# Optimization experiments

Measured on AMD Instinct MI355X. Metric: run time of the kernel, lower is better.

## Reference

```python
import jax, jax.numpy as jnp
import numpy as np

H = 128          # hidden_dim
L = 3            # num_layers
EPS = 1e-5       # BatchNorm eps


def setup_inputs() -> dict:
    key = jax.random.key(0)
    ks = jax.random.split(key, 12)
    B, N = 32, 8192
    s = 0.05
    x = jax.random.normal(ks[0], (B, N, 2), dtype=jnp.float32)
    mask = jnp.ones((B, N), dtype=jnp.float32)
    # parameters, stored as [in, out]
    emb_w = jax.random.normal(ks[1], (2, H), jnp.float32) * s
    emb_b = jnp.zeros((H,), jnp.float32)
    lin_w = jax.random.normal(ks[2], (L, H, H), jnp.float32) * s
    lin_b = jnp.zeros((L, H), jnp.float32)
    nb_w = jax.random.normal(ks[3], (L, H, H), jnp.float32) * s
    nb_b = jnp.zeros((L, H), jnp.float32)
    bn_g = jnp.ones((L, H), jnp.float32)
    bn_b = jnp.zeros((L, H), jnp.float32)
    out1_w = jax.random.normal(ks[4], (H, H // 2), jnp.float32) * s
    out1_b = jnp.zeros((H // 2,), jnp.float32)
    out2_w = jax.random.normal(ks[5], (H // 2, 2), jnp.float32) * s
    out2_b = jnp.zeros((2,), jnp.float32)
    return dict(x=x, mask=mask, emb_w=emb_w, emb_b=emb_b,
                lin_w=lin_w, lin_b=lin_b, nb_w=nb_w, nb_b=nb_b,
                bn_g=bn_g, bn_b=bn_b, out1_w=out1_w, out1_b=out1_b,
                out2_w=out2_w, out2_b=out2_b)


def reference(x, mask, emb_w, emb_b, lin_w, lin_b, nb_w, nb_b,
              bn_g, bn_b, out1_w, out1_b, out2_w, out2_b):
    m = mask[..., None]                     # [B, N, 1]
    h = x @ emb_w + emb_b                   # [B, N, H]
    for i in range(L):
        # graph conv: self transform + ring-neighbor (roll) transform
        nsum = jnp.roll(h, 1, axis=1) + jnp.roll(h, -1, axis=1)
        h_new = (h @ lin_w[i] + lin_b[i] + nsum @ nb_w[i] + nb_b[i]) * m
        # BatchNorm1d (training-mode batch stats over batch*nodes per channel)
        mean = jnp.mean(h_new, axis=(0, 1))
        var = jnp.mean(jnp.square(h_new - mean), axis=(0, 1))  # biased var
        h_new = (h_new - mean) * jax.lax.rsqrt(var + EPS) * bn_g[i] + bn_b[i]
        h_new = jax.nn.relu(h_new)          # dropout treated as identity (eval)
        h = h + h_new                       # residual
    out = jax.nn.relu(h @ out1_w + out1_b) @ out2_w + out2_b  # [B, N, 2]
    return out * m
```

## Files before the change

### kernel.cpp

```cpp
#include <hip/hip_runtime.h>
#include <cstddef>

#define H      128
#define NBATCH 32
#define NN     8192
#define RTOT   (NBATCH*NN)
#define NLAYER 3
#define BNEPS  1e-5f
#define NSLOT  16
#define CNPB   128
#define NTILEC (RTOT/CNPB)
#define HNPB   64
#define HS_STRIDE 136

typedef _Float16 f16;
typedef __attribute__((ext_vector_type(8))) _Float16 half8;
typedef __attribute__((ext_vector_type(4))) float f32x4;

__device__ __forceinline__ void unpackh8(uint4 pk, float* d) {
    const f16* hp = (const f16*)&pk;
    #pragma unroll
    for (int i = 0; i < 8; ++i) d[i] = (float)hp[i];
}
__device__ __forceinline__ uint4 packh8(const float* s) {
    uint4 pk;
    f16* hp = (f16*)&pk;
    #pragma unroll
    for (int i = 0; i < 8; ++i) hp[i] = (f16)s[i];
    return pk;
}

__device__ __forceinline__ void load_bfrags(
    const f16* __restrict__ Wt, half8 bW[2][4], int colbase, int l15, int quad)
{
    #pragma unroll
    for (int nt = 0; nt < 2; ++nt) {
        int nrow = colbase + nt * 16 + l15;
        #pragma unroll
        for (int ks = 0; ks < 4; ++ks)
            bW[nt][ks] = *((const half8*)(Wt + nrow * 128 + ks * 32 + quad * 8));
    }
}

__device__ __forceinline__ void conv_mfma8(
    const f16* __restrict__ hs, const half8 bWl[2][4], const half8 bWn[2][4],
    f32x4 acc[8][2], int l15, int quad)
{
    #pragma unroll
    for (int mt = 0; mt < 8; ++mt) {
        acc[mt][0] = (f32x4){0.f, 0.f, 0.f, 0.f};
        acc[mt][1] = (f32x4){0.f, 0.f, 0.f, 0.f};
    }
    #pragma unroll
    for (int ks = 0; ks < 4; ++ks) {
        #pragma unroll
        for (int mt = 0; mt < 8; ++mt) {
            int row = mt * 16 + l15;
            const f16* base = hs + row * HS_STRIDE + ks * 32 + quad * 8;
            half8 hm = *((const half8*)(base + HS_STRIDE));
            half8 hd = *((const half8*)(base));
            half8 hu = *((const half8*)(base + 2 * HS_STRIDE));
            half8 an = hd + hu;
            acc[mt][0] = __builtin_amdgcn_mfma_f32_16x16x32_f16(hm, bWl[0][ks], acc[mt][0], 0, 0, 0);
            acc[mt][1] = __builtin_amdgcn_mfma_f32_16x16x32_f16(hm, bWl[1][ks], acc[mt][1], 0, 0, 0);
            acc[mt][0] = __builtin_amdgcn_mfma_f32_16x16x32_f16(an, bWn[0][ks], acc[mt][0], 0, 0, 0);
            acc[mt][1] = __builtin_amdgcn_mfma_f32_16x16x32_f16(an, bWn[1][ks], acc[mt][1], 0, 0, 0);
        }
    }
}

__global__ __launch_bounds__(256) void k_prep(
    const float* __restrict__ lin_w, const float* __restrict__ nb_w,
    f16* __restrict__ Wlt, f16* __restrict__ Wnt)
{
    int id = blockIdx.x * 256 + threadIdx.x;
    int mat = id / 49152;
    int r   = id - mat * 49152;
    int l   = r >> 14;
    int r2  = r & 16383;
    int k   = r2 >> 7;
    int n   = r2 & 127;
    const float* src = mat ? nb_w : lin_w;
    f16*         dst = mat ? Wnt  : Wlt;
    dst[l * 16384 + n * 128 + k] = (f16)src[l * 16384 + k * 128 + n];
}

__device__ __forceinline__ void conv_epilogue_c(
    f32x4 acc[8][2], const float bsum[2], const float* __restrict__ msk,
    f16* __restrict__ hnb, float* __restrict__ gstats,
    int tile, int wave, int quad, int lane, int slot)
{
    uint2* out2 = (uint2*)hnb;
    float s[2] = {0.f, 0.f}, ss[2] = {0.f, 0.f};
    #pragma unroll
    for (int nt = 0; nt < 2; ++nt) {
        #pragma unroll
        for (int mt = 0; mt < 8; ++mt) {
            f16 v4[4];
            #pragma unroll
            for (int reg = 0; reg < 4; ++reg) {
                int lrow = mt * 16 + quad * 4 + reg;
                float v = (acc[mt][nt][reg] + bsum[nt]) * msk[lrow];
                v4[reg] = (f16)v;
                s[nt] += v; ss[nt] += v * v;
            }
            size_t chunk = ((size_t)tile * 4 + wave) * 16 + mt * 2 + nt;
            out2[chunk * 64 + lane] = *((const uint2*)v4);
        }
    }
    #pragma unroll
    for (int nt = 0; nt < 2; ++nt) {
        s[nt]  += __shfl_xor(s[nt], 16);  s[nt]  += __shfl_xor(s[nt], 32);
        ss[nt] += __shfl_xor(ss[nt], 16); ss[nt] += __shfl_xor(ss[nt], 32);
    }
    if (lane < 16) {
        int colbase = wave * 32;
        #pragma unroll
        for (int nt = 0; nt < 2; ++nt) {
            int col = colbase + nt * 16 + lane;
            atomicAdd(&gstats[slot * 2 * H + col],     s[nt]);
            atomicAdd(&gstats[slot * 2 * H + H + col], ss[nt]);
        }
    }
}

__global__ __launch_bounds__(256) void k_conv0f(
    const float* __restrict__ x, const float* __restrict__ ew,
    const float* __restrict__ eb,
    const f16* __restrict__ Wlt, const f16* __restrict__ Wnt,
    const float* __restrict__ bl, const float* __restrict__ bnb,
    const float* __restrict__ mask,
    f16* __restrict__ hnb, float* __restrict__ gstats)
{
    __shared__ __align__(16) f16 hs[(CNPB + 2) * HS_STRIDE];
    __shared__ float ews[3 * H], msk[CNPB];
    const int t = threadIdx.x, lane = t & 63;
    const int l15 = lane & 15, quad = lane >> 4;
    const int wave = t >> 6;
    const int colbase = wave * 32;
    const int r0 = blockIdx.x * CNPB;
    const int batch = r0 >> 13, n0 = r0 & (NN - 1);

    half8 bWl[2][4], bWn[2][4];
    load_bfrags(Wlt, bWl, colbase, l15, quad);
    load_bfrags(Wnt, bWn, colbase, l15, quad);
    float bsum[2];
    #pragma unroll
    for (int nt = 0; nt < 2; ++nt) {
        int col = colbase + nt * 16 + l15;
        bsum[nt] = bl[col] + bnb[col];
    }
    for (int c = t; c < H; c += 256) {
        ews[c] = ew[c]; ews[H + c] = ew[H + c]; ews[2 * H + c] = eb[c];
    }
    if (t < CNPB) msk[t] = mask[r0 + t];
    __syncthreads();

    for (int i = t; i < (CNPB + 2) * 16; i += 256) {
        int row = i >> 4, g = i & 15;
        int n = (n0 + row - 1 + NN) & (NN - 1);
        const float* xp = x + 2 * ((size_t)batch * NN + n);
        float x0 = xp[0], x1 = xp[1];
        f16 o[8];
        #pragma unroll
        for (int e = 0; e < 8; ++e) {
            int c = g * 8 + e;
            o[e] = (f16)fmaf(x1, ews[H + c], fmaf(x0, ews[c], ews[2 * H + c]));
        }
        *((uint4*)(hs + row * HS_STRIDE + g * 8)) = *((const uint4*)o);
    }
    __syncthreads();

    f32x4 acc[8][2];
    conv_mfma8(hs, bWl, bWn, acc, l15, quad);

    conv_epilogue_c(acc, bsum, msk, hnb, gstats,
                    blockIdx.x, wave, quad, lane, blockIdx.x & (NSLOT - 1));
}

__global__ __launch_bounds__(256) void k_conv(
    const f16* __restrict__ hb,
    const f16* __restrict__ Wlt, const f16* __restrict__ Wnt,
    const float* __restrict__ bl, const float* __restrict__ bnb,
    const float* __restrict__ mask,
    f16* __restrict__ hnb, float* __restrict__ gstats)
{
    __shared__ __align__(16) f16 hs[(CNPB + 2) * HS_STRIDE];
    __shared__ float msk[CNPB];
    const int t = threadIdx.x, lane = t & 63;
    const int l15 = lane & 15, quad = lane >> 4;
    const int wave = t >> 6;
    const int colbase = wave * 32;
    const int r0 = blockIdx.x * CNPB;
    const int batch = r0 >> 13, n0 = r0 & (NN - 1);

    half8 bWl[2][4], bWn[2][4];
    load_bfrags(Wlt, bWl, colbase, l15, quad);
    load_bfrags(Wnt, bWn, colbase, l15, quad);
    float bsum[2];
    #pragma unroll
    for (int nt = 0; nt < 2; ++nt) {
        int col = colbase + nt * 16 + l15;
        bsum[nt] = bl[col] + bnb[col];
    }
    if (t < CNPB) msk[t] = mask[r0 + t];

    for (int i = t; i < (CNPB + 2) * 16; i += 256) {
        int row = i >> 4, g = i & 15;
        int n = (n0 + row - 1 + NN) & (NN - 1);
        *((uint4*)(hs + row * HS_STRIDE + g * 8)) =
            *((const uint4*)(hb + ((size_t)(batch * NN + n)) * H + g * 8));
    }
    __syncthreads();

    f32x4 acc[8][2];
    conv_mfma8(hs, bWl, bWn, acc, l15, quad);

    conv_epilogue_c(acc, bsum, msk, hnb, gstats,
                    blockIdx.x, wave, quad, lane, blockIdx.x & (NSLOT - 1));
}

__device__ __forceinline__ void norm_ingest(
    const f16* __restrict__ hnb, int blk, int t,
    const float* __restrict__ scl_s, const float* __restrict__ sft_s,
    f16* __restrict__ g)
{
    const uint4* src = (const uint4*)hnb + (size_t)blk * 2048;
    for (int i = t; i < 2048; i += 256) {
        uint4 pk = src[i];
        int chunk = i >> 5;
        int L     = (i & 31) * 2;
        int ntv   = chunk & 1;
        int mtv   = (chunk >> 1) & 7;
        int wv    = chunk >> 4;
        int c0    = wv * 32 + ntv * 16 + (L & 15);
        int row0  = mtv * 16 + (L >> 4) * 4;
        float vv[8];
        unpackh8(pk, vv);
        #pragma unroll
        for (int e = 0; e < 8; ++e) {
            int cc = c0 + (e >> 2);
            int rr = row0 + (e & 3);
            float q = fmaxf(fmaf(vv[e], scl_s[cc], sft_s[cc]), 0.f);
            g[rr * HS_STRIDE + cc] = (f16)q;
        }
    }
}

__device__ __forceinline__ void bn_finalize(
    const float* __restrict__ gstats, const float* __restrict__ bn_g,
    const float* __restrict__ bn_b, int t, float* scl_s, float* sft_s)
{
    if (t < H) {
        float s = 0.f, ss = 0.f;
        #pragma unroll
        for (int i = 0; i < NSLOT; ++i) {
            s  += gstats[i * 2 * H + t];
            ss += gstats[i * 2 * H + H + t];
        }
        const float invR = 1.f / (float)RTOT;
        float mean = s * invR;
        float var  = ss * invR - mean * mean;
        float inv  = rsqrtf(var + BNEPS);
        float sc   = bn_g[t] * inv;
        scl_s[t] = sc;
        sft_s[t] = fmaf(-mean, sc, bn_b[t]);
    }
}

__global__ __launch_bounds__(256) void k_norm0(
    const float* __restrict__ x, const float* __restrict__ ew,
    const float* __restrict__ eb, const f16* __restrict__ hnb,
    const float* __restrict__ gstats, const float* __restrict__ bn_g,
    const float* __restrict__ bn_b, f16* __restrict__ hb)
{
    __shared__ __align__(16) f16 g[CNPB * HS_STRIDE];
    __shared__ float scl_s[H], sft_s[H], ews[3 * H];
    const int t = threadIdx.x;
    const int blk = blockIdx.x;
    const size_t r0 = (size_t)blk * CNPB;

    bn_finalize(gstats, bn_g, bn_b, t, scl_s, sft_s);
    if (t < H) { ews[t] = ew[t]; ews[H + t] = ew[H + t]; ews[2 * H + t] = eb[t]; }
    __syncthreads();

    norm_ingest(hnb, blk, t, scl_s, sft_s, g);
    __syncthreads();

    for (int i = t; i < 2048; i += 256) {
        int row = i >> 4, gg = i & 15;
        size_t grow = r0 + row;
        float x0 = x[2 * grow], x1 = x[2 * grow + 1];
        uint4 pg = *((const uint4*)(g + row * HS_STRIDE + gg * 8));
        float vg[8], vh[8];
        unpackh8(pg, vg);
        #pragma unroll
        for (int e = 0; e < 8; ++e) {
            int c = gg * 8 + e;
            float h0 = fmaf(x1, ews[H + c], fmaf(x0, ews[c], ews[2 * H + c]));
            vh[e] = h0 + vg[e];
        }
        *((uint4*)(hb + grow * H + gg * 8)) = packh8(vh);
    }
}

__global__ __launch_bounds__(256) void k_norm(
    const f16* __restrict__ hnb, const float* __restrict__ gstats,
    const float* __restrict__ bn_g, const float* __restrict__ bn_b,
    f16* __restrict__ hb)
{
    __shared__ __align__(16) f16 g[CNPB * HS_STRIDE];
    __shared__ float scl_s[H], sft_s[H];
    const int t = threadIdx.x;
    const int blk = blockIdx.x;
    const size_t r0 = (size_t)blk * CNPB;

    bn_finalize(gstats, bn_g, bn_b, t, scl_s, sft_s);
    __syncthreads();

    norm_ingest(hnb, blk, t, scl_s, sft_s, g);
    __syncthreads();

    for (int i = t; i < 2048; i += 256) {
        int row = i >> 4, gg = i & 15;
        size_t grow = r0 + row;
        uint4 ph = *((const uint4*)(hb + grow * H + gg * 8));
        uint4 pg = *((const uint4*)(g + row * HS_STRIDE + gg * 8));
        float vh[8], vg[8];
        unpackh8(ph, vh);
        unpackh8(pg, vg);
        #pragma unroll
        for (int e = 0; e < 8; ++e) vh[e] += vg[e];
        *((uint4*)(hb + grow * H + gg * 8)) = packh8(vh);
    }
}

__global__ __launch_bounds__(256) void k_head(
    const f16* __restrict__ hb, const float* __restrict__ W1,
    const float* __restrict__ b1, const float* __restrict__ W2,
    const float* __restrict__ b2, const float* __restrict__ mask,
    float* __restrict__ out)
{
    __shared__ f16 hs [64 * HS_STRIDE];
    __shared__ f16 w1t[64 * HS_STRIDE];
    const int t    = threadIdx.x;
    const int wave = t >> 6;
    const int lane = t & 63;
    const int l15  = lane & 15;
    const int quad = lane >> 4;
    const int r0   = blockIdx.x * HNPB;

    for (int i = t; i < 64 * 16; i += 256) {
        int row = i >> 4, g = i & 15;
        *((uint4*)(hs + row * HS_STRIDE + g * 8)) =
            *((const uint4*)(hb + (size_t)(r0 + row) * H + g * 8));
    }
    for (int i = t; i < H * 64; i += 256) {
        int k = i >> 6, n = i & 63;
        w1t[n * HS_STRIDE + k] = (f16)W1[i];
    }
    __syncthreads();

    f32x4 acc[4];
    #pragma unroll
    for (int nt = 0; nt < 4; ++nt) acc[nt] = (f32x4){0.f, 0.f, 0.f, 0.f};

    #pragma unroll
    for (int ks = 0; ks < 4; ++ks) {
        half8 a = *((const half8*)(hs + (wave * 16 + l15) * HS_STRIDE + ks * 32 + quad * 8));
        #pragma unroll
        for (int nt = 0; nt < 4; ++nt) {
            half8 b = *((const half8*)(w1t + (nt * 16 + l15) * HS_STRIDE + ks * 32 + quad * 8));
            acc[nt] = __builtin_amdgcn_mfma_f32_16x16x32_f16(a, b, acc[nt], 0, 0, 0);
        }
    }

    float p0[4] = {0,0,0,0}, p1[4] = {0,0,0,0};
    #pragma unroll
    for (int nt = 0; nt < 4; ++nt) {
        int col = nt * 16 + l15;
        float bb = b1[col];
        float wa = W2[2 * col], wb = W2[2 * col + 1];
        #pragma unroll
        for (int reg = 0; reg < 4; ++reg) {
            float v = fmaxf(acc[nt][reg] + bb, 0.f);
            p0[reg] = fmaf(v, wa, p0[reg]);
            p1[reg] = fmaf(v, wb, p1[reg]);
        }
    }
    #pragma unroll
    for (int reg = 0; reg < 4; ++reg) {
        p0[reg] += __shfl_xor(p0[reg], 1); p0[reg] += __shfl_xor(p0[reg], 2);
        p0[reg] += __shfl_xor(p0[reg], 4); p0[reg] += __shfl_xor(p0[reg], 8);
        p1[reg] += __shfl_xor(p1[reg], 1); p1[reg] += __shfl_xor(p1[reg], 2);
        p1[reg] += __shfl_xor(p1[reg], 4); p1[reg] += __shfl_xor(p1[reg], 8);
    }
    if (l15 == 0) {
        #pragma unroll
        for (int reg = 0; reg < 4; ++reg) {
            int gr = r0 + wave * 16 + quad * 4 + reg;
            float m = mask[gr];
            float2 o;
            o.x = (p0[reg] + b2[0]) * m;
            o.y = (p1[reg] + b2[1]) * m;
            *((float2*)(out + 2 * gr)) = o;
        }
    }
}

extern "C" void kernel_launch(void* const* d_in, const int* in_sizes, int n_in,
                              void* d_out, int out_size, void* d_ws, size_t ws_size,
                              hipStream_t stream)
{
    const float* x     = (const float*)d_in[0];
    const float* mask  = (const float*)d_in[1];
    const float* emb_w = (const float*)d_in[2];
    const float* emb_b = (const float*)d_in[3];
    const float* lin_w = (const float*)d_in[4];
    const float* lin_b = (const float*)d_in[5];
    const float* nb_w  = (const float*)d_in[6];
    const float* nb_b  = (const float*)d_in[7];
    const float* bn_g  = (const float*)d_in[8];
    const float* bn_b  = (const float*)d_in[9];
    const float* o1w   = (const float*)d_in[10];
    const float* o1b   = (const float*)d_in[11];
    const float* o2w   = (const float*)d_in[12];
    const float* o2b   = (const float*)d_in[13];
    float* out = (float*)d_out;

    char* ws = (char*)d_ws;
    f16* hb  = (f16*)ws;
    f16* hnb = (f16*)(ws + (size_t)RTOT * H * 2);

    float* gst = (float*)d_out;
    f16* Wlt = (f16*)((float*)d_out + 65536);
    f16* Wnt = Wlt + NLAYER * H * H;

    hipMemsetAsync(gst, 0, NLAYER * NSLOT * 2 * H * sizeof(float), stream);
    k_prep<<<384, 256, 0, stream>>>(lin_w, nb_w, Wlt, Wnt);

    k_conv0f<<<NTILEC, 256, 0, stream>>>(
        x, emb_w, emb_b, Wlt, Wnt, lin_b, nb_b, mask, hnb, gst);
    k_norm0<<<NTILEC, 256, 0, stream>>>(
        x, emb_w, emb_b, hnb, gst, bn_g, bn_b, hb);

    for (int i = 1; i < NLAYER; ++i) {
        k_conv<<<NTILEC, 256, 0, stream>>>(
            hb, Wlt + i * H * H, Wnt + i * H * H,
            lin_b + i * H, nb_b + i * H, mask,
            hnb, gst + i * NSLOT * 2 * H);
        k_norm<<<NTILEC, 256, 0, stream>>>(
            hnb, gst + i * NSLOT * 2 * H, bn_g + i * H, bn_b + i * H, hb);
    }
    k_head<<<RTOT / HNPB, 256, 0, stream>>>(hb, o1w, o1b, o2w, o2b, mask, out);
}
```

Baseline: 343.6 us.

## Fuse BatchNorm apply and residual into next conv's load and head

Removes the separate normalize kernels. Each conv kernel now rebuilds its input tile from the previous pre-norm activations and a tiny per-channel scale/shift buffer computed by a one-block finalize kernel. The epilogue stages results through shared memory to write row-major tiles with coalesced stores. This saves a full read and write pass per layer. In exchange, halo rows are recomputed, and the path needs a third workspace buffer, so it only runs when the workspace size check passes.

```diff
diff --git a/kernel.cpp b/kernel.cpp
--- a/kernel.cpp
+++ b/kernel.cpp
@@ -124,6 +124,45 @@
     }
 }
 
+__device__ __forceinline__ void conv_epilogue_rm(
+    f32x4 acc[8][2], const float bsum[2], const float* __restrict__ msk,
+    f16* __restrict__ tr, f16* __restrict__ hnb, float* __restrict__ gstats,
+    int r0, int colbase, int l15, int quad, int lane, int t, int slot)
+{
+    float s[2] = {0.f, 0.f}, ss[2] = {0.f, 0.f};
+    #pragma unroll
+    for (int nt = 0; nt < 2; ++nt) {
+        int col = colbase + nt * 16 + l15;
+        #pragma unroll
+        for (int mt = 0; mt < 8; ++mt)
+            #pragma unroll
+            for (int reg = 0; reg < 4; ++reg) {
+                int lrow = mt * 16 + quad * 4 + reg;
+                float v = (acc[mt][nt][reg] + bsum[nt]) * msk[lrow];
+                tr[lrow * HS_STRIDE + col] = (f16)v;
+                s[nt] += v; ss[nt] += v * v;
+            }
+    }
+    #pragma unroll
+    for (int nt = 0; nt < 2; ++nt) {
+        s[nt]  += __shfl_xor(s[nt], 16);  s[nt]  += __shfl_xor(s[nt], 32);
+        ss[nt] += __shfl_xor(ss[nt], 16); ss[nt] += __shfl_xor(ss[nt], 32);
+    }
+    if (lane < 16)
+        #pragma unroll
+        for (int nt = 0; nt < 2; ++nt) {
+            int col = colbase + nt * 16 + lane;
+            atomicAdd(&gstats[slot * 2 * H + col],     s[nt]);
+            atomicAdd(&gstats[slot * 2 * H + H + col], ss[nt]);
+        }
+    __syncthreads();
+    for (int i = t; i < CNPB * 16; i += 256) {
+        int row = i >> 4, g = i & 15;
+        *((uint4*)(hnb + (size_t)(r0 + row) * H + g * 8)) =
+            *((const uint4*)(tr + row * HS_STRIDE + g * 8));
+    }
+}
+
 __global__ __launch_bounds__(256) void k_conv0f(
     const float* __restrict__ x, const float* __restrict__ ew,
     const float* __restrict__ eb,
@@ -173,9 +212,62 @@
 
     f32x4 acc[8][2];
     conv_mfma8(hs, bWl, bWn, acc, l15, quad);
-
     conv_epilogue_c(acc, bsum, msk, hnb, gstats,
                     blockIdx.x, wave, quad, lane, blockIdx.x & (NSLOT - 1));
+}
+
+__global__ __launch_bounds__(256) void k_conv0f_rm(
+    const float* __restrict__ x, const float* __restrict__ ew,
+    const float* __restrict__ eb,
+    const f16* __restrict__ Wlt, const f16* __restrict__ Wnt,
+    const float* __restrict__ bl, const float* __restrict__ bnb,
+    const float* __restrict__ mask,
+    f16* __restrict__ hnb, float* __restrict__ gstats)
+{
+    __shared__ __align__(16) f16 hs[(CNPB + 2) * HS_STRIDE];
+    __shared__ float ews[3 * H], msk[CNPB];
+    const int t = threadIdx.x, lane = t & 63;
+    const int l15 = lane & 15, quad = lane >> 4;
+    const int wave = t >> 6;
+    const int colbase = wave * 32;
+    const int r0 = blockIdx.x * CNPB;
+    const int batch = r0 >> 13, n0 = r0 & (NN - 1);
+
+    half8 bWl[2][4], bWn[2][4];
+    load_bfrags(Wlt, bWl, colbase, l15, quad);
+    load_bfrags(Wnt, bWn, colbase, l15, quad);
+    float bsum[2];
+    #pragma unroll
+    for (int nt = 0; nt < 2; ++nt) {
+        int col = colbase + nt * 16 + l15;
+        bsum[nt] = bl[col] + bnb[col];
+    }
+    for (int c = t; c < H; c += 256) {
+        ews[c] = ew[c]; ews[H + c] = ew[H + c]; ews[2 * H + c] = eb[c];
+    }
+    if (t < CNPB) msk[t] = mask[r0 + t];
+    __syncthreads();
+
+    for (int i = t; i < (CNPB + 2) * 16; i += 256) {
+        int row = i >> 4, g = i & 15;
+        int n = (n0 + row - 1 + NN) & (NN - 1);
+        const float* xp = x + 2 * ((size_t)batch * NN + n);
+        float x0 = xp[0], x1 = xp[1];
+        f16 o[8];
+        #pragma unroll
+        for (int e = 0; e < 8; ++e) {
+            int c = g * 8 + e;
+            o[e] = (f16)fmaf(x1, ews[H + c], fmaf(x0, ews[c], ews[2 * H + c]));
+        }
+        *((uint4*)(hs + row * HS_STRIDE + g * 8)) = *((const uint4*)o);
+    }
+    __syncthreads();
+
+    f32x4 acc[8][2];
+    conv_mfma8(hs, bWl, bWn, acc, l15, quad);
+    __syncthreads();
+    conv_epilogue_rm(acc, bsum, msk, hs, hnb, gstats,
+                     r0, colbase, l15, quad, lane, t, blockIdx.x & (NSLOT - 1));
 }
 
 __global__ __launch_bounds__(256) void k_conv(
@@ -215,9 +307,154 @@
 
     f32x4 acc[8][2];
     conv_mfma8(hs, bWl, bWn, acc, l15, quad);
-
     conv_epilogue_c(acc, bsum, msk, hnb, gstats,
                     blockIdx.x, wave, quad, lane, blockIdx.x & (NSLOT - 1));
+}
+
+__global__ __launch_bounds__(256) void k_cn1(
+    const float* __restrict__ x, const float* __restrict__ ew,
+    const float* __restrict__ eb, const f16* __restrict__ hnA,
+    const float* __restrict__ scl0,
+    const f16* __restrict__ Wlt, const f16* __restrict__ Wnt,
+    const float* __restrict__ bl, const float* __restrict__ bnb,
+    const float* __restrict__ mask,
+    f16* __restrict__ HB, f16* __restrict__ hnB, float* __restrict__ gst1)
+{
+    __shared__ __align__(16) f16 hs[(CNPB + 2) * HS_STRIDE];
+    __shared__ float ews[3 * H], sclA[2 * H], msk[CNPB];
+    const int t = threadIdx.x, lane = t & 63;
+    const int l15 = lane & 15, quad = lane >> 4;
+    const int wave = t >> 6;
+    const int colbase = wave * 32;
+    const int r0 = blockIdx.x * CNPB;
+    const int batch = r0 >> 13, n0 = r0 & (NN - 1);
+
+    half8 bWl[2][4], bWn[2][4];
+    load_bfrags(Wlt, bWl, colbase, l15, quad);
+    load_bfrags(Wnt, bWn, colbase, l15, quad);
+    float bsum[2];
+    #pragma unroll
+    for (int nt = 0; nt < 2; ++nt) {
+        int col = colbase + nt * 16 + l15;
+        bsum[nt] = bl[col] + bnb[col];
+    }
+    for (int c = t; c < H; c += 256) {
+        ews[c] = ew[c]; ews[H + c] = ew[H + c]; ews[2 * H + c] = eb[c];
+        sclA[c] = scl0[c]; sclA[H + c] = scl0[H + c];
+    }
+    if (t < CNPB) msk[t] = mask[r0 + t];
+    __syncthreads();
+
+    for (int i = t; i < (CNPB + 2) * 16; i += 256) {
+        int row = i >> 4, g = i & 15;
+        int n = (n0 + row - 1 + NN) & (NN - 1);
+        size_t base = (size_t)batch * NN + n;
+        const float* xp = x + 2 * base;
+        float x0 = xp[0], x1 = xp[1];
+        uint4 pa = *((const uint4*)(hnA + base * H + g * 8));
+        float va[8];
+        unpackh8(pa, va);
+        f16 o[8];
+        #pragma unroll
+        for (int e = 0; e < 8; ++e) {
+            int c = g * 8 + e;
+            float h0 = fmaf(x1, ews[H + c], fmaf(x0, ews[c], ews[2 * H + c]));
+            o[e] = (f16)(h0 + fmaxf(fmaf(va[e], sclA[c], sclA[H + c]), 0.f));
+        }
+        *((uint4*)(hs + row * HS_STRIDE + g * 8)) = *((const uint4*)o);
+    }
+    __syncthreads();
+
+    f32x4 acc[8][2];
+    conv_mfma8(hs, bWl, bWn, acc, l15, quad);
+
+    for (int i = t; i < CNPB * 16; i += 256) {
+        int row = i >> 4, g = i & 15;
+        *((uint4*)(HB + (size_t)(r0 + row) * H + g * 8)) =
+            *((const uint4*)(hs + (row + 1) * HS_STRIDE + g * 8));
+    }
+    __syncthreads();
+
+    conv_epilogue_rm(acc, bsum, msk, hs, hnB, gst1,
+                     r0, colbase, l15, quad, lane, t, blockIdx.x & (NSLOT - 1));
+}
+
+__global__ __launch_bounds__(256) void k_cn2(
+    const f16* __restrict__ HB, const f16* __restrict__ hnB,
+    const float* __restrict__ scl1,
+    const f16* __restrict__ Wlt, const f16* __restrict__ Wnt,
+    const float* __restrict__ bl, const float* __restrict__ bnb,
+    const float* __restrict__ mask,
+    f16* __restrict__ hnA, float* __restrict__ gst2)
+{
+    __shared__ __align__(16) f16 hs[(CNPB + 2) * HS_STRIDE];
+    __shared__ float sclA[2 * H], msk[CNPB];
+    const int t = threadIdx.x, lane = t & 63;
+    const int l15 = lane & 15, quad = lane >> 4;
+    const int wave = t >> 6;
+    const int colbase = wave * 32;
+    const int r0 = blockIdx.x * CNPB;
+    const int batch = r0 >> 13, n0 = r0 & (NN - 1);
+
+    half8 bWl[2][4], bWn[2][4];
+    load_bfrags(Wlt, bWl, colbase, l15, quad);
+    load_bfrags(Wnt, bWn, colbase, l15, quad);
+    float bsum[2];
+    #pragma unroll
+    for (int nt = 0; nt < 2; ++nt) {
+        int col = colbase + nt * 16 + l15;
+        bsum[nt] = bl[col] + bnb[col];
+    }
+    for (int c = t; c < H; c += 256) {
+        sclA[c] = scl1[c]; sclA[H + c] = scl1[H + c];
+    }
+    if (t < CNPB) msk[t] = mask[r0 + t];
+    __syncthreads();
+
+    for (int i = t; i < (CNPB + 2) * 16; i += 256) {
+        int row = i >> 4, g = i & 15;
+        int n = (n0 + row - 1 + NN) & (NN - 1);
+        size_t off = ((size_t)batch * NN + n) * H + g * 8;
+        uint4 ph = *((const uint4*)(HB + off));
+        uint4 pn = *((const uint4*)(hnB + off));
+        float vh[8], vn[8];
+        unpackh8(ph, vh);
+        unpackh8(pn, vn);
+        f16 o[8];
+        #pragma unroll
+        for (int e = 0; e < 8; ++e) {
+            int c = g * 8 + e;
+            o[e] = (f16)(vh[e] + fmaxf(fmaf(vn[e], sclA[c], sclA[H + c]), 0.f));
+        }
+        *((uint4*)(hs + row * HS_STRIDE + g * 8)) = *((const uint4*)o);
+    }
+    __syncthreads();
+
+    f32x4 acc[8][2];
+    conv_mfma8(hs, bWl, bWn, acc, l15, quad);
+    __syncthreads();
+
+    conv_epilogue_rm(acc, bsum, msk, hs, hnA, gst2,
+                     r0, colbase, l15, quad, lane, t, blockIdx.x & (NSLOT - 1));
+}
+
+__global__ void k_fin(const float* __restrict__ gstats,
+                      const float* __restrict__ g, const float* __restrict__ b,
+                      float* __restrict__ o)
+{
+    int c = threadIdx.x;
+    float s = 0.f, ss = 0.f;
+    for (int i = 0; i < NSLOT; ++i) {
+        s  += gstats[i * 2 * H + c];
+        ss += gstats[i * 2 * H + H + c];
+    }
+    const float invR = 1.f / (float)RTOT;
+    float mean = s * invR;
+    float var  = ss * invR - mean * mean;
+    float inv  = rsqrtf(var + BNEPS);
+    float sc   = g[c] * inv;
+    o[c] = sc;
+    o[H + c] = fmaf(-mean, sc, b[c]);
 }
 
 __device__ __forceinline__ void norm_ingest(
@@ -364,7 +601,6 @@
     f32x4 acc[4];
     #pragma unroll
     for (int nt = 0; nt < 4; ++nt) acc[nt] = (f32x4){0.f, 0.f, 0.f, 0.f};
-
     #pragma unroll
     for (int ks = 0; ks < 4; ++ks) {
         half8 a = *((const half8*)(hs + (wave * 16 + l15) * HS_STRIDE + ks * 32 + quad * 8));
@@ -403,6 +639,97 @@
             float2 o;
             o.x = (p0[reg] + b2[0]) * m;
             o.y = (p1[reg] + b2[1]) * m;
+            *((float2*)(out + 2 * gr)) = o;
+        }
+    }
+}
+
+__global__ __launch_bounds__(256) void k_head_f(
+    const f16* __restrict__ HB, const f16* __restrict__ hn1,
+    const f16* __restrict__ hn2, const float* __restrict__ sclb,
+    const float* __restrict__ W1, const float* __restrict__ b1,
+    const float* __restrict__ W2, const float* __restrict__ b2,
+    const float* __restrict__ mask, float* __restrict__ out)
+{
+    __shared__ f16 hs [64 * HS_STRIDE];
+    __shared__ f16 w1t[64 * HS_STRIDE];
+    __shared__ float sclA[4 * H];
+    const int t    = threadIdx.x;
+    const int wave = t >> 6;
+    const int lane = t & 63;
+    const int l15  = lane & 15;
+    const int quad = lane >> 4;
+    const int r0   = blockIdx.x * HNPB;
+
+    for (int i = t; i < 4 * H; i += 256) sclA[i] = sclb[i];
+    for (int i = t; i < H * 64; i += 256) {
+        int k = i >> 6, n = i & 63;
+        w1t[n * HS_STRIDE + k] = (f16)W1[i];
+    }
+    __syncthreads();
+
+    for (int i = t; i < 64 * 16; i += 256) {
+        int row = i >> 4, g = i & 15;
+        size_t off = (size_t)(r0 + row) * H + g * 8;
+        uint4 ph = *((const uint4*)(HB + off));
+        uint4 p1v = *((const uint4*)(hn1 + off));
+        uint4 p2v = *((const uint4*)(hn2 + off));
+        float vh[8], v1[8], v2[8];
+        unpackh8(ph, vh);
+        unpackh8(p1v, v1);
+        unpackh8(p2v, v2);
+        f16 o[8];
+        #pragma unroll
+        for (int e = 0; e < 8; ++e) {
+            int c = g * 8 + e;
+            float h2 = vh[e] + fmaxf(fmaf(v1[e], sclA[c],         sclA[H + c]),     0.f);
+            o[e] = (f16)(h2 + fmaxf(fmaf(v2[e], sclA[2 * H + c], sclA[3 * H + c]), 0.f));
+        }
+        *((uint4*)(hs + row * HS_STRIDE + g * 8)) = *((const uint4*)o);
+    }
+    __syncthreads();
+
+    f32x4 acc[4];
+    #pragma unroll
+    for (int nt = 0; nt < 4; ++nt) acc[nt] = (f32x4){0.f, 0.f, 0.f, 0.f};
+    #pragma unroll
+    for (int ks = 0; ks < 4; ++ks) {
+        half8 a = *((const half8*)(hs + (wave * 16 + l15) * HS_STRIDE + ks * 32 + quad * 8));
+        #pragma unroll
+        for (int nt = 0; nt < 4; ++nt) {
+            half8 b = *((const half8*)(w1t + (nt * 16 + l15) * HS_STRIDE + ks * 32 + quad * 8));
+            acc[nt] = __builtin_amdgcn_mfma_f32_16x16x32_f16(a, b, acc[nt], 0, 0, 0);
+        }
+    }
+
+    float p0[4] = {0,0,0,0}, p1a[4] = {0,0,0,0};
+    #pragma unroll
+    for (int nt = 0; nt < 4; ++nt) {
+        int col = nt * 16 + l15;
+        float bb = b1[col];
+        float wa = W2[2 * col], wb = W2[2 * col + 1];
+        #pragma unroll
+        for (int reg = 0; reg < 4; ++reg) {
+            float v = fmaxf(acc[nt][reg] + bb, 0.f);
+            p0[reg]  = fmaf(v, wa, p0[reg]);
+            p1a[reg] = fmaf(v, wb, p1a[reg]);
+        }
+    }
+    #pragma unroll
+    for (int reg = 0; reg < 4; ++reg) {
+        p0[reg]  += __shfl_xor(p0[reg], 1);  p0[reg]  += __shfl_xor(p0[reg], 2);
+        p0[reg]  += __shfl_xor(p0[reg], 4);  p0[reg]  += __shfl_xor(p0[reg], 8);
+        p1a[reg] += __shfl_xor(p1a[reg], 1); p1a[reg] += __shfl_xor(p1a[reg], 2);
+        p1a[reg] += __shfl_xor(p1a[reg], 4); p1a[reg] += __shfl_xor(p1a[reg], 8);
+    }
+    if (l15 == 0) {
+        #pragma unroll
+        for (int reg = 0; reg < 4; ++reg) {
+            int gr = r0 + wave * 16 + quad * 4 + reg;
+            float m = mask[gr];
+            float2 o;
+            o.x = (p0[reg]  + b2[0]) * m;
+            o.y = (p1a[reg] + b2[1]) * m;
             *((float2*)(out + 2 * gr)) = o;
         }
     }
@@ -428,9 +755,8 @@
     const float* o2b   = (const float*)d_in[13];
     float* out = (float*)d_out;
 
+    const size_t BUF = (size_t)RTOT * H * 2;
     char* ws = (char*)d_ws;
-    f16* hb  = (f16*)ws;
-    f16* hnb = (f16*)(ws + (size_t)RTOT * H * 2);
 
     float* gst = (float*)d_out;
     f16* Wlt = (f16*)((float*)d_out + 65536);
@@ -439,18 +765,43 @@
     hipMemsetAsync(gst, 0, NLAYER * NSLOT * 2 * H * sizeof(float), stream);
     k_prep<<<384, 256, 0, stream>>>(lin_w, nb_w, Wlt, Wnt);
 
-    k_conv0f<<<NTILEC, 256, 0, stream>>>(
-        x, emb_w, emb_b, Wlt, Wnt, lin_b, nb_b, mask, hnb, gst);
-    k_norm0<<<NTILEC, 256, 0, stream>>>(
-        x, emb_w, emb_b, hnb, gst, bn_g, bn_b, hb);
-
-    for (int i = 1; i < NLAYER; ++i) {
-        k_conv<<<NTILEC, 256, 0, stream>>>(
-            hb, Wlt + i * H * H, Wnt + i * H * H,
-            lin_b + i * H, nb_b + i * H, mask,
-            hnb, gst + i * NSLOT * 2 * H);
-        k_norm<<<NTILEC, 256, 0, stream>>>(
-            hnb, gst + i * NSLOT * 2 * H, bn_g + i * H, bn_b + i * H, hb);
-    }
-    k_head<<<RTOT / HNPB, 256, 0, stream>>>(hb, o1w, o1b, o2w, o2b, mask, out);
-}
+    if (ws_size >= 3 * BUF + 65536) {
+        f16* HB  = (f16*)ws;
+        f16* hnA = (f16*)(ws + BUF);
+        f16* hnB = (f16*)(ws + 2 * BUF);
+        float* sclbuf = (float*)(ws + 3 * BUF);
+
+        k_conv0f_rm<<<NTILEC, 256, 0, stream>>>(
+            x, emb_w, emb_b, Wlt, Wnt, lin_b, nb_b, mask, hnA, gst);
+        k_fin<<<1, H, 0, stream>>>(gst, bn_g, bn_b, sclbuf);
+        k_cn1<<<NTILEC, 256, 0, stream>>>(
+            x, emb_w, emb_b, hnA, sclbuf, Wlt + H * H, Wnt + H * H,
+            lin_b + H, nb_b + H, mask, HB, hnB, gst + NSLOT * 2 * H);
+        k_fin<<<1, H, 0, stream>>>(gst + NSLOT * 2 * H, bn_g + H, bn_b + H,
+                                   sclbuf + 2 * H);
+        k_cn2<<<NTILEC, 256, 0, stream>>>(
+            HB, hnB, sclbuf + 2 * H, Wlt + 2 * H * H, Wnt + 2 * H * H,
+            lin_b + 2 * H, nb_b + 2 * H, mask, hnA, gst + 2 * NSLOT * 2 * H);
+        k_fin<<<1, H, 0, stream>>>(gst + 2 * NSLOT * 2 * H, bn_g + 2 * H,
+                                   bn_b + 2 * H, sclbuf + 4 * H);
+        k_head_f<<<RTOT / HNPB, 256, 0, stream>>>(
+            HB, hnB, hnA, sclbuf + 2 * H, o1w, o1b, o2w, o2b, mask, out);
+    } else {
+        f16* hb  = (f16*)ws;
+        f16* hnb = (f16*)(ws + BUF);
+
+        k_conv0f<<<NTILEC, 256, 0, stream>>>(
+            x, emb_w, emb_b, Wlt, Wnt, lin_b, nb_b, mask, hnb, gst);
+        k_norm0<<<NTILEC, 256, 0, stream>>>(
+            x, emb_w, emb_b, hnb, gst, bn_g, bn_b, hb);
+        for (int i = 1; i < NLAYER; ++i) {
+            k_conv<<<NTILEC, 256, 0, stream>>>(
+                hb, Wlt + i * H * H, Wnt + i * H * H,
+                lin_b + i * H, nb_b + i * H, mask,
+                hnb, gst + i * NSLOT * 2 * H);
+            k_norm<<<NTILEC, 256, 0, stream>>>(
+                hnb, gst + i * NSLOT * 2 * H, bn_g + i * H, bn_b + i * H, hb);
+        }
+        k_head<<<RTOT / HNPB, 256, 0, stream>>>(hb, o1w, o1b, o2w, o2b, mask, out);
+    }
+}
```

New measurement: 323.7 us. -5.8%, faster.
